# Kernel optimization log

Hardware: AMD Instinct MI355X
Metric: run time of the kernel (lower is better)

## Reference

```python
import jax, jax.numpy as jnp
import numpy as np

B, T, C, H = 2, 2048, 2048, 32
N = C // H  # 64
EPS_GN = 1e-5 * 8 ** 2  # eps = 1e-5 * head_size_divisor**2


def setup_inputs() -> dict:
    key = jax.random.key(0)
    ks = jax.random.split(key, 40)
    p = lambda i, shape, s=1.0: jax.random.normal(ks[i], shape, jnp.float32) * s
    inp = {
        'x': p(0, (B, T, C)),
        'shift_state': jnp.zeros((B, C), jnp.float32),
        'v_first': p(1, (B, T, C)),
        'wkv_state': jnp.zeros((B, H, N, N), jnp.float32),
        # token-shift mix coefficients [1,1,C]
        'x_r': p(2, (1, 1, C), 0.3), 'x_w': p(3, (1, 1, C), 0.3),
        'x_k': p(4, (1, 1, C), 0.3), 'x_v': p(5, (1, 1, C), 0.3),
        'x_a': p(6, (1, 1, C), 0.3), 'x_g': p(7, (1, 1, C), 0.3),
        # decay LoRA
        'w0': p(8, (1, 1, C), 0.5) - 4.0,
        'w1': p(9, (C, 64), 0.02), 'w2': p(10, (64, C), 0.02),
        # in-context-learning-rate LoRA
        'a0': p(11, (1, 1, C), 0.1),
        'a1': p(12, (C, 64), 0.02), 'a2': p(13, (64, C), 0.02),
        # value-mix LoRA
        'v0': p(14, (1, 1, C), 0.1) + 1.0,
        'v1': p(15, (C, 32), 0.02), 'v2': p(16, (32, C), 0.02),
        # gate LoRA
        'g1': p(17, (C, 128), 0.02), 'g2': p(18, (128, C), 0.02),
        'k_k': p(19, (1, 1, C), 0.05) + 0.85,
        'k_a': p(20, (1, 1, C), 0.05) + 1.0,
        'r_k': p(21, (H, N), 0.1),
        # dense projections (applied as x @ W.T like nn.Linear)
        'Wr': p(22, (C, C), 0.02), 'Wk': p(23, (C, C), 0.02),
        'Wv': p(24, (C, C), 0.02), 'Wo': p(25, (C, C), 0.02),
        'ln_w': jnp.ones((C,), jnp.float32),
        'ln_b': jnp.zeros((C,), jnp.float32),
    }
    return inp


def reference(x, shift_state, v_first, wkv_state, x_r, x_w, x_k, x_v, x_a, x_g,
              w0, w1, w2, a0, a1, a2, v0, v1, v2, g1, g2, k_k, k_a, r_k,
              Wr, Wk, Wv, Wo, ln_w, ln_b):
    # token shift: xx[t] = x[t-1] - x[t] (prev from shift_state at t=0)
    xx = jnp.concatenate([shift_state[:, None, :], x[:, :-1]], axis=1) - x
    xr, xw, xk, xv, xa, xg = (x + xx * m for m in (x_r, x_w, x_k, x_v, x_a, x_g))

    r = xr @ Wr.T
    w = -jax.nn.softplus(-(w0 + jnp.tanh(xw @ w1) @ w2)) - 0.5  # log-decay in (-inf,-0.5)
    k = xk @ Wk.T
    v = xv @ Wv.T
    v = v + (v_first - v) * jax.nn.sigmoid(v0 + (xv @ v1) @ v2)  # layer_id > 0 branch
    a = jax.nn.sigmoid(a0 + (xa @ a1) @ a2)
    g = jax.nn.sigmoid(xg @ g1) @ g2

    kk = (k * k_k).reshape(B, T, H, N)
    kk = kk / jnp.maximum(jnp.linalg.norm(kk, axis=-1, keepdims=True), 1e-12)
    kk = kk.reshape(B, T, C)
    k = k * (1.0 + (a - 1.0) * k_a)

    # RWKV-7 generalized delta-rule recurrence (a_in=-kk, b_in=kk*a):
    #   S_t = S_{t-1} * diag(exp(w_t)) + (S_{t-1} a_t) b_t^T + v_t k_t^T ; o_t = S_t r_t
    to_tbhn = lambda z: z.reshape(B, T, H, N).transpose(1, 0, 2, 3)  # [T,B,H,N]
    rs, ws, ks, vs, as_, bs = map(to_tbhn, (r, w, k, v, -kk, kk * a))

    def step(S, ins):  # S: [B,H,N,N] indexed [v_dim, k_dim]
        r_t, w_t, k_t, v_t, a_t, b_t = ins
        sa = jnp.einsum('bhij,bhj->bhi', S, a_t)
        S = (S * jnp.exp(w_t)[:, :, None, :]
             + sa[..., None] * b_t[:, :, None, :]
             + v_t[..., None] * k_t[:, :, None, :])
        o_t = jnp.einsum('bhij,bhj->bhi', S, r_t)
        return S, o_t

    _, o = jax.lax.scan(step, wkv_state, (rs, ws, ks, vs, as_, bs))  # o: [T,B,H,N]
    o = o.transpose(1, 0, 2, 3).reshape(B, T, C)

    # GroupNorm with H groups over channel dim
    og = o.reshape(B, T, H, N)
    mu = og.mean(-1, keepdims=True)
    var = og.var(-1, keepdims=True)
    o = ((og - mu) / jnp.sqrt(var + EPS_GN)).reshape(B, T, C) * ln_w + ln_b

    # bonus term
    rk = (r.reshape(B, T, H, N) * k.reshape(B, T, H, N) * r_k).sum(-1, keepdims=True)
    o = o + (rk * v.reshape(B, T, H, N)).reshape(B, T, C)

    return (o * g) @ Wo.T
```

## Files before the change

kernel.cpp:

```cpp
#include <hip/hip_runtime.h>

#define Bdim 2
#define Tdim 2048
#define Cdim 2048
#define Hdim 32
#define Mdim (Bdim*Tdim)

typedef unsigned short u16;
typedef short bf16x8 __attribute__((ext_vector_type(8)));
typedef short bf16x4 __attribute__((ext_vector_type(4)));
typedef float f32x4 __attribute__((ext_vector_type(4)));

__device__ __forceinline__ u16 f2bf(float f) {
  unsigned u = __float_as_uint(f);
  u = (u + 0x7FFFu + ((u >> 16) & 1u)) >> 16;
  return (u16)u;
}
__device__ __forceinline__ float b2f(u16 h) {
  return __uint_as_float(((unsigned)h) << 16);
}
__device__ __forceinline__ float sigf(float x) { return 1.f / (1.f + expf(-x)); }

__device__ __forceinline__ void gld16(const u16* g, u16* l) {
  __builtin_amdgcn_global_load_lds(
      (const __attribute__((address_space(1))) unsigned int*)g,
      (__attribute__((address_space(3))) unsigned int*)l, 16, 0, 0);
}

__device__ __forceinline__ float dpp_red16(float x) {
  int t = __builtin_amdgcn_mov_dpp(__float_as_int(x), 0x128, 0xF, 0xF, true);
  x += __int_as_float(t);
  t = __builtin_amdgcn_mov_dpp(__float_as_int(x), 0x124, 0xF, 0xF, true);
  x += __int_as_float(t);
  t = __builtin_amdgcn_mov_dpp(__float_as_int(x), 0x122, 0xF, 0xF, true);
  x += __int_as_float(t);
  t = __builtin_amdgcn_mov_dpp(__float_as_int(x), 0x121, 0xF, 0xF, true);
  x += __int_as_float(t);
  return x;
}

__global__ __launch_bounds__(256) void fill_kernel(float* __restrict__ out, float v, int n) {
  int i = blockIdx.x * 256 + threadIdx.x;
  if (i < n) out[i] = v;
}

__global__ __launch_bounds__(256) void prep_kernel(
    const float* __restrict__ x, const float* __restrict__ shift,
    const float* __restrict__ mr, const float* __restrict__ mw,
    const float* __restrict__ mk, const float* __restrict__ mv,
    const float* __restrict__ ma, const float* __restrict__ mg,
    u16* __restrict__ xr_h, u16* __restrict__ xr_l,
    u16* __restrict__ xk_h, u16* __restrict__ xk_l,
    u16* __restrict__ xv_h, u16* __restrict__ xv_l,
    u16* __restrict__ xg_h, u16* __restrict__ xg_l,
    u16* __restrict__ xw, u16* __restrict__ xa)
{
  size_t idx = (size_t)blockIdx.x * 256 + threadIdx.x;
  int c = (int)(idx & (Cdim - 1));
  size_t row = idx >> 11;
  int t = (int)(row & (Tdim - 1));
  int b = (int)(row >> 11);
  float xc = x[idx];
  float xp = (t == 0) ? shift[(size_t)b * Cdim + c] : x[idx - Cdim];
  float xx = xp - xc;

  float vr = xc + xx * mr[c];
  u16 hr = f2bf(vr); xr_h[idx] = hr; xr_l[idx] = f2bf(vr - b2f(hr));
  float vk = xc + xx * mk[c];
  u16 hk = f2bf(vk); xk_h[idx] = hk; xk_l[idx] = f2bf(vk - b2f(hk));
  float vv = xc + xx * mv[c];
  u16 hv = f2bf(vv); xv_h[idx] = hv; xv_l[idx] = f2bf(vv - b2f(hv));
  float vg = xc + xx * mg[c];
  u16 hg = f2bf(vg); xg_h[idx] = hg; xg_l[idx] = f2bf(vg - b2f(hg));

  xw[idx] = f2bf(xc + xx * mw[c]);
  xa[idx] = f2bf(xc + xx * ma[c]);
}

__global__ __launch_bounds__(256) void cast_split_kernel(
    const float* __restrict__ src, u16* __restrict__ hi, u16* __restrict__ lo)
{
  size_t i = (size_t)blockIdx.x * 256 + threadIdx.x;
  float v = src[i];
  u16 h = f2bf(v);
  hi[i] = h;
  lo[i] = f2bf(v - b2f(h));
}

__global__ __launch_bounds__(256) void transpose_pack_kernel(
    const float* __restrict__ src, u16* __restrict__ dst, int K, int Nsrc)
{
  size_t idx = (size_t)blockIdx.x * 256 + threadIdx.x;
  int n = (int)(idx / K);
  int kk = (int)(idx - (size_t)n * K);
  dst[idx] = (n < Nsrc) ? f2bf(src[(size_t)kk * Nsrc + n]) : (u16)0;
}

__global__ __launch_bounds__(256) void transpose_pack_split_kernel(
    const float* __restrict__ src, u16* __restrict__ dh, u16* __restrict__ dl,
    int K, int Nsrc)
{
  size_t idx = (size_t)blockIdx.x * 256 + threadIdx.x;
  int n = (int)(idx / K);
  int kk = (int)(idx - (size_t)n * K);
  float v = (n < Nsrc) ? src[(size_t)kk * Nsrc + n] : 0.f;
  u16 h = f2bf(v);
  dh[idx] = h;
  dl[idx] = f2bf(v - b2f(h));
}


template <int EP>
__device__ __forceinline__ void gemm_plain_body(
    const u16* __restrict__ A, const u16* __restrict__ B, void* __restrict__ Cv,
    const float* __restrict__ bias, const float* __restrict__ aux1,
    const float* __restrict__ aux2, int K, int Nact, int ldC, int act)
{
  __shared__ u16 As[128][32];
  __shared__ u16 Bs[128][32];
  int tid = threadIdx.x;
  int lane = tid & 63, wave = tid >> 6;
  int wm = wave >> 1, wn = wave & 1;
  int bm = blockIdx.x * 128, bn = blockIdx.y * 128;
  f32x4 zero = {0.f, 0.f, 0.f, 0.f};
  f32x4 acc[4][4];
#pragma unroll
  for (int i = 0; i < 4; i++)
#pragma unroll
    for (int j = 0; j < 4; j++) acc[i][j] = zero;
  int srow = tid >> 2;
  int sslot = tid & 3;
  int scol = (sslot ^ (srow & 3)) << 3;
  int dcol = sslot << 3;
  const u16* gA  = A + (size_t)(bm + srow) * K + scol;
  const u16* gA2 = A + (size_t)(bm + 64 + srow) * K + scol;
  const u16* gB  = B + (size_t)(bn + srow) * K + scol;
  const u16* gB2 = B + (size_t)(bn + 64 + srow) * K + scol;
  u16* lA  = &As[srow][dcol];
  u16* lA2 = &As[64 + srow][dcol];
  u16* lB  = &Bs[srow][dcol];
  u16* lB2 = &Bs[64 + srow][dcol];
  int fr = lane & 15;
  int fk = ((lane >> 4) << 3) ^ ((fr & 3) << 3);
  for (int k0 = 0; k0 < K; k0 += 32) {
    __syncthreads();
    gld16(gA + k0, lA);
    gld16(gA2 + k0, lA2);
    gld16(gB + k0, lB);
    gld16(gB2 + k0, lB2);
    __syncthreads();
    bf16x8 af[4], bfv[4];
#pragma unroll
    for (int i = 0; i < 4; i++) af[i] = *(const bf16x8*)&As[wm * 64 + i * 16 + fr][fk];
#pragma unroll
    for (int j = 0; j < 4; j++) bfv[j] = *(const bf16x8*)&Bs[wn * 64 + j * 16 + fr][fk];
#pragma unroll
    for (int i = 0; i < 4; i++)
#pragma unroll
      for (int j = 0; j < 4; j++)
        acc[i][j] = __builtin_amdgcn_mfma_f32_16x16x32_bf16(af[i], bfv[j], acc[i][j], 0, 0, 0);
  }
  int rb = (lane >> 4) << 2;
  int cc = lane & 15;
#pragma unroll
  for (int i = 0; i < 4; i++) {
    int mm = bm + wm * 64 + i * 16 + rb;
#pragma unroll
    for (int j = 0; j < 4; j++) {
      int nn = bn + wn * 64 + j * 16 + cc;
      if (nn < Nact) {
#pragma unroll
        for (int r = 0; r < 4; r++) {
          float val = acc[i][j][r];
          size_t oidx = (size_t)(mm + r) * ldC + nn;
          if (EP == 1) ((u16*)Cv)[oidx] = f2bf(tanhf(val));
          else if (EP == 2) {
            if (act == 1) val = tanhf(val);
            ((u16*)Cv)[oidx] = f2bf(val);
          }
          else if (EP == 3) ((u16*)Cv)[oidx] = f2bf(0.60653065971f * sigf(bias[nn] + val));
          else if (EP == 4) ((float*)Cv)[oidx] = sigf(bias[nn] + val);
          else if (EP == 5) {
            float vraw = aux1[oidx], vf = aux2[oidx];
            ((float*)Cv)[oidx] = vraw + (vf - vraw) * sigf(bias[nn] + val);
          }
        }
      }
    }
  }
}

template <int EP>
__global__ __launch_bounds__(256) void gemm_plain(
    const u16* __restrict__ A, const u16* __restrict__ B, void* __restrict__ C,
    const float* __restrict__ bias, const float* __restrict__ aux1,
    const float* __restrict__ aux2, int K, int Nact, int ldC)
{
  gemm_plain_body<EP>(A, B, C, bias, aux1, aux2, K, Nact, ldC, 0);
}

__global__ __launch_bounds__(256) void lora1_kernel(
    const u16* A0, const u16* A1, const u16* A2,
    const u16* B0, const u16* B1, const u16* B2,
    u16* C0, u16* C1, u16* C2, int N0, int N1, int N2)
{
  int z = blockIdx.z;
  const u16* A = (z == 0) ? A0 : (z == 1) ? A1 : A2;
  const u16* B = (z == 0) ? B0 : (z == 1) ? B1 : B2;
  u16* C      = (z == 0) ? C0 : (z == 1) ? C1 : C2;
  int Nact    = (z == 0) ? N0 : (z == 1) ? N1 : N2;
  int act     = (z == 0) ? 1 : 0;
  gemm_plain_body<2>(A, B, C, nullptr, nullptr, nullptr, 2048, Nact, Nact, act);
}

template <int EP>
__global__ __launch_bounds__(256) void gemm_split(
    const u16* __restrict__ Ah, const u16* __restrict__ Al,
    const u16* __restrict__ Bh, const u16* __restrict__ Bl,
    void* __restrict__ C1, u16* __restrict__ C2, int K, int Nact, int ldC)
{
  __shared__ u16 Ash[128][32];
  __shared__ u16 Asl[128][32];
  __shared__ u16 Bsh[128][32];
  __shared__ u16 Bsl[128][32];
  int tid = threadIdx.x;
  int lane = tid & 63, wave = tid >> 6;
  int wm = wave >> 1, wn = wave & 1;
  int bm = blockIdx.x * 128, bn = blockIdx.y * 128;
  f32x4 zero = {0.f, 0.f, 0.f, 0.f};
  f32x4 acc[4][4];
#pragma unroll
  for (int i = 0; i < 4; i++)
#pragma unroll
    for (int j = 0; j < 4; j++) acc[i][j] = zero;
  int srow = tid >> 2;
  int sslot = tid & 3;
  int scol = (sslot ^ (srow & 3)) << 3;
  int dcol = sslot << 3;
  size_t ga  = (size_t)(bm + srow) * K + scol;
  size_t ga2 = (size_t)(bm + 64 + srow) * K + scol;
  size_t gb  = (size_t)(bn + srow) * K + scol;
  size_t gb2 = (size_t)(bn + 64 + srow) * K + scol;
  u16* lAh = &Ash[srow][dcol];  u16* lAh2 = &Ash[64 + srow][dcol];
  u16* lAl = &Asl[srow][dcol];  u16* lAl2 = &Asl[64 + srow][dcol];
  u16* lBh = &Bsh[srow][dcol];  u16* lBh2 = &Bsh[64 + srow][dcol];
  u16* lBl = &Bsl[srow][dcol];  u16* lBl2 = &Bsl[64 + srow][dcol];
  int fr = lane & 15;
  int fk = ((lane >> 4) << 3) ^ ((fr & 3) << 3);
  for (int k0 = 0; k0 < K; k0 += 32) {
    __syncthreads();
    gld16(Ah + ga + k0, lAh);
    gld16(Ah + ga2 + k0, lAh2);
    gld16(Al + ga + k0, lAl);
    gld16(Al + ga2 + k0, lAl2);
    gld16(Bh + gb + k0, lBh);
    gld16(Bh + gb2 + k0, lBh2);
    gld16(Bl + gb + k0, lBl);
    gld16(Bl + gb2 + k0, lBl2);
    __syncthreads();
    bf16x8 fah[4], fal[4], fbh[4], fbl[4];
#pragma unroll
    for (int i = 0; i < 4; i++) {
      fah[i] = *(const bf16x8*)&Ash[wm * 64 + i * 16 + fr][fk];
      fal[i] = *(const bf16x8*)&Asl[wm * 64 + i * 16 + fr][fk];
    }
#pragma unroll
    for (int j = 0; j < 4; j++) {
      fbh[j] = *(const bf16x8*)&Bsh[wn * 64 + j * 16 + fr][fk];
      fbl[j] = *(const bf16x8*)&Bsl[wn * 64 + j * 16 + fr][fk];
    }
#pragma unroll
    for (int i = 0; i < 4; i++)
#pragma unroll
      for (int j = 0; j < 4; j++) {
        acc[i][j] = __builtin_amdgcn_mfma_f32_16x16x32_bf16(fah[i], fbh[j], acc[i][j], 0, 0, 0);
        acc[i][j] = __builtin_amdgcn_mfma_f32_16x16x32_bf16(fah[i], fbl[j], acc[i][j], 0, 0, 0);
        acc[i][j] = __builtin_amdgcn_mfma_f32_16x16x32_bf16(fal[i], fbh[j], acc[i][j], 0, 0, 0);
      }
  }
  int rb = (lane >> 4) << 2;
  int cc = lane & 15;
#pragma unroll
  for (int i = 0; i < 4; i++) {
    int mm = bm + wm * 64 + i * 16 + rb;
#pragma unroll
    for (int j = 0; j < 4; j++) {
      int nn = bn + wn * 64 + j * 16 + cc;
      if (nn < Nact) {
#pragma unroll
        for (int r = 0; r < 4; r++) {
          float val = acc[i][j][r];
          size_t oidx = (size_t)(mm + r) * ldC + nn;
          if (EP == 0) ((float*)C1)[oidx] = val;
          else {
            float s = sigf(val);
            u16 h = f2bf(s);
            ((u16*)C1)[oidx] = h;
            C2[oidx] = f2bf(s - b2f(h));
          }
        }
      }
    }
  }
}

__global__ __launch_bounds__(256) void post_kernel(
    float* __restrict__ k, const float* __restrict__ a,
    const float* __restrict__ k_k, const float* __restrict__ k_a,
    float* __restrict__ ain, float* __restrict__ bin)
{
  int gid = blockIdx.x * 4 + (threadIdx.x >> 6);
  int lane = threadIdx.x & 63;
  int m = gid >> 5, h = gid & 31;
  int c = h * 64 + lane;
  size_t idx = (size_t)m * Cdim + c;

  float kr = k[idx];
  float av = a[idx];

  float kkv = kr * k_k[c];
  float ss = kkv * kkv;
#pragma unroll
  for (int off = 32; off; off >>= 1) ss += __shfl_xor(ss, off);
  float kkn = kkv / fmaxf(sqrtf(ss), 1e-12f);

  ain[idx] = -kkn;
  bin[idx] = kkn * av;
  k[idx] = kr * (1.f + (av - 1.f) * k_a[c]);
}

__global__ __launch_bounds__(64) void scan_kernel(
    const float* __restrict__ r, const u16* __restrict__ ew,
    const float* __restrict__ k, const float* __restrict__ v,
    const float* __restrict__ ain, const float* __restrict__ bin,
    const float* __restrict__ S0, float* __restrict__ o)
{
  int bh = blockIdx.x & 63;
  int rg = blockIdx.x >> 6;
  int lane = threadIdx.x;
  int c16 = lane & 15;
  int lr = lane >> 4;
  int i = rg * 4 + lr;
  int cb = (bh & 31) * 64;
  size_t mbase = (size_t)(bh >> 5) * Tdim;

  float s[4];
  {
    const float* sp = S0 + (size_t)bh * 4096 + (size_t)i * 64 + c16 * 4;
#pragma unroll
    for (int j = 0; j < 4; j++) s[j] = sp[j];
  }

  f32x4 aA, kA, bA, rA;  bf16x4 eA;  float vA;
  f32x4 aB, kB, bB, rB;  bf16x4 eB;  float vB;
  f32x4 aC, kC, bC, rC;  bf16x4 eC;  float vC;
  f32x4 aD, kD, bD, rD;  bf16x4 eD;  float vD;

#define PRE(tt, P) { \
  size_t vb_ = (mbase + (size_t)(tt)) * Cdim + cb; \
  a##P = *(const f32x4*)(ain + vb_ + c16 * 4); \
  k##P = *(const f32x4*)(k + vb_ + c16 * 4); \
  b##P = *(const f32x4*)(bin + vb_ + c16 * 4); \
  r##P = *(const f32x4*)(r + vb_ + c16 * 4); \
  e##P = *(const bf16x4*)(ew + vb_ + c16 * 4); \
  v##P = v[vb_ + i]; }

#define COMP(tt, P) { \
  float p0_ = s[0] * a##P[0] + s[1] * a##P[1]; \
  float p1_ = s[2] * a##P[2] + s[3] * a##P[3]; \
  float p_ = dpp_red16(p0_ + p1_); \
  float oL_ = 0.f, oH_ = 0.f; \
  _Pragma("unroll") \
  for (int j = 0; j < 2; j++) { \
    float sn0_ = s[j]     * b2f((u16)e##P[j])     + p_ * b##P[j]     + v##P * k##P[j]; \
    float sn1_ = s[2 + j] * b2f((u16)e##P[2 + j]) + p_ * b##P[2 + j] + v##P * k##P[2 + j]; \
    s[j] = sn0_; s[2 + j] = sn1_; \
    oL_ += sn0_ * r##P[j]; oH_ += sn1_ * r##P[2 + j]; \
  } \
  float oo_ = dpp_red16(oL_ + oH_); \
  if (c16 == 0) o[(mbase + (size_t)(tt)) * Cdim + cb + i] = oo_; \
  __builtin_amdgcn_sched_barrier(0); }

  PRE(0, A)
  PRE(1, B)
  PRE(2, C)
  for (int t = 0; t < Tdim - 4; t += 4) {
    PRE(t + 3, D)
    COMP(t, A)
    PRE(t + 4, A)
    COMP(t + 1, B)
    PRE(t + 5, B)
    COMP(t + 2, C)
    PRE(t + 6, C)
    COMP(t + 3, D)
  }
  PRE(Tdim - 1, D)
  COMP(Tdim - 4, A)
  COMP(Tdim - 3, B)
  COMP(Tdim - 2, C)
  COMP(Tdim - 1, D)
#undef PRE
#undef COMP
}

__global__ __launch_bounds__(256) void gn_kernel(
    const float* __restrict__ o_raw, const float* __restrict__ r,
    const float* __restrict__ k, const float* __restrict__ v,
    const float* __restrict__ g, const float* __restrict__ rkw,
    const float* __restrict__ ln_w, const float* __restrict__ ln_b,
    u16* __restrict__ og_h, u16* __restrict__ og_l)
{
  int gid = blockIdx.x * 4 + (threadIdx.x >> 6);
  int lane = threadIdx.x & 63;
  int m = gid >> 5, h = gid & 31;
  int c = h * 64 + lane;
  size_t idx = (size_t)m * Cdim + c;

  float ov = o_raw[idx];
  float rv = r[idx], kv = k[idx], vv = v[idx];
  float rk = rv * kv * rkw[c];

  float s1 = ov, s2 = ov * ov, s3 = rk;
#pragma unroll
  for (int off = 32; off; off >>= 1) {
    s1 += __shfl_xor(s1, off);
    s2 += __shfl_xor(s2, off);
    s3 += __shfl_xor(s3, off);
  }
  float mu = s1 * (1.f / 64.f);
  float var = s2 * (1.f / 64.f) - mu * mu;
  float xh = (ov - mu) * rsqrtf(var + 6.4e-4f);
  float gn = xh * ln_w[c] + ln_b[c];
  float outp = (gn + s3 * vv) * g[idx];
  u16 hh = f2bf(outp);
  og_h[idx] = hh;
  og_l[idx] = f2bf(outp - b2f(hh));
}

extern "C" void kernel_launch(void* const* d_in, const int* in_sizes, int n_in,
                              void* d_out, int out_size, void* d_ws, size_t ws_size,
                              hipStream_t stream) {
  const float* x      = (const float*)d_in[0];
  const float* shiftS = (const float*)d_in[1];
  const float* vfirst = (const float*)d_in[2];
  const float* wkv0   = (const float*)d_in[3];
  const float* x_r = (const float*)d_in[4];
  const float* x_w = (const float*)d_in[5];
  const float* x_k = (const float*)d_in[6];
  const float* x_v = (const float*)d_in[7];
  const float* x_a = (const float*)d_in[8];
  const float* x_g = (const float*)d_in[9];
  const float* w0 = (const float*)d_in[10];
  const float* w1 = (const float*)d_in[11];
  const float* w2 = (const float*)d_in[12];
  const float* a0 = (const float*)d_in[13];
  const float* a1 = (const float*)d_in[14];
  const float* a2 = (const float*)d_in[15];
  const float* v0 = (const float*)d_in[16];
  const float* v1 = (const float*)d_in[17];
  const float* v2 = (const float*)d_in[18];
  const float* g1 = (const float*)d_in[19];
  const float* g2 = (const float*)d_in[20];
  const float* k_k = (const float*)d_in[21];
  const float* k_a = (const float*)d_in[22];
  const float* r_k = (const float*)d_in[23];
  const float* Wr = (const float*)d_in[24];
  const float* Wk = (const float*)d_in[25];
  const float* Wv = (const float*)d_in[26];
  const float* Wo = (const float*)d_in[27];
  const float* ln_w = (const float*)d_in[28];
  const float* ln_b = (const float*)d_in[29];
  (void)in_sizes; (void)n_in;

  const size_t MC = (size_t)Mdim * Cdim;
  const size_t CC = (size_t)Cdim * Cdim;
  const size_t SLOT = MC * 2;

  char* cur = (char*)d_ws;
  auto alloc = [&](size_t bytes) -> void* {
    void* p = cur;
    cur += (bytes + 255) & ~(size_t)255;
    return p;
  };

  char* X = (char*)alloc(13 * SLOT);
  u16* xr_h = (u16*)(X + 0 * SLOT);
  u16* xr_l = (u16*)(X + 1 * SLOT);
  u16* xk_h = (u16*)(X + 2 * SLOT);
  u16* xk_l = (u16*)(X + 3 * SLOT);
  u16* xv_h = (u16*)(X + 4 * SLOT);
  u16* xv_l = (u16*)(X + 5 * SLOT);
  u16* xw   = (u16*)(X + 6 * SLOT);
  u16* xa   = (u16*)(X + 7 * SLOT);
  u16* xg_h = (u16*)(X + 8 * SLOT);
  u16* xg_l = (u16*)(X + 9 * SLOT);
  float* r_f32 = (float*)(X + 8 * SLOT);
  float* k_f32 = (float*)(X + 0 * SLOT);
  float* v_f32 = (float*)(X + 2 * SLOT);
  float* a_f32 = (float*)(X + 10 * SLOT);
  u16*   ew_bf = (u16*)(X + 12 * SLOT);
  float* ain_f = (float*)(X + 4 * SLOT);
  float* bin_f = (float*)(X + 6 * SLOT);
  float* o_f32 = (float*)(X + 10 * SLOT);
  float* g_f32 = (float*)(X + 6 * SLOT);
  u16*   og_h  = (u16*)(X + 4 * SLOT);
  u16*   og_l  = (u16*)(X + 5 * SLOT);

  u16* Wh = (u16*)alloc(CC * 2);
  u16* Wl = (u16*)alloc(CC * 2);

  u16* w1t = (u16*)alloc((size_t)128 * 2048 * 2);
  u16* a1t = (u16*)alloc((size_t)128 * 2048 * 2);
  u16* v1t = (u16*)alloc((size_t)128 * 2048 * 2);
  u16* g1t_h = (u16*)alloc((size_t)128 * 2048 * 2);
  u16* g1t_l = (u16*)alloc((size_t)128 * 2048 * 2);
  u16* w2t = (u16*)alloc((size_t)2048 * 64 * 2);
  u16* a2t = (u16*)alloc((size_t)2048 * 64 * 2);
  u16* v2t = (u16*)alloc((size_t)2048 * 32 * 2);
  u16* g2t_h = (u16*)alloc((size_t)2048 * 128 * 2);
  u16* g2t_l = (u16*)alloc((size_t)2048 * 128 * 2);
  u16* hb_w = (u16*)alloc((size_t)Mdim * 64 * 2);
  u16* hb_a = (u16*)alloc((size_t)Mdim * 64 * 2);
  u16* hb_v = (u16*)alloc((size_t)Mdim * 32 * 2);
  u16* sig_h = (u16*)alloc((size_t)Mdim * 128 * 2);
  u16* sig_l = (u16*)alloc((size_t)Mdim * 128 * 2);

  size_t required = (size_t)(cur - (char*)d_ws);
  if (ws_size < required) {
    fill_kernel<<<(out_size + 255) / 256, 256, 0, stream>>>(
        (float*)d_out, (float)(ws_size >> 20), out_size);
    return;
  }

  prep_kernel<<<(int)(MC / 256), 256, 0, stream>>>(
      x, shiftS, x_r, x_w, x_k, x_v, x_a, x_g,
      xr_h, xr_l, xk_h, xk_l, xv_h, xv_l, xg_h, xg_l, xw, xa);

  transpose_pack_kernel<<<1024, 256, 0, stream>>>(w1, w1t, 2048, 64);
  transpose_pack_kernel<<<1024, 256, 0, stream>>>(a1, a1t, 2048, 64);
  transpose_pack_kernel<<<1024, 256, 0, stream>>>(v1, v1t, 2048, 32);
  transpose_pack_split_kernel<<<1024, 256, 0, stream>>>(g1, g1t_h, g1t_l, 2048, 128);
  transpose_pack_kernel<<<512, 256, 0, stream>>>(w2, w2t, 64, 2048);
  transpose_pack_kernel<<<512, 256, 0, stream>>>(a2, a2t, 64, 2048);
  transpose_pack_kernel<<<256, 256, 0, stream>>>(v2, v2t, 32, 2048);
  transpose_pack_split_kernel<<<1024, 256, 0, stream>>>(g2, g2t_h, g2t_l, 128, 2048);

  dim3 gL1(Mdim / 128, 1, 3);
  lora1_kernel<<<gL1, 256, 0, stream>>>(xw, xa, xv_h, w1t, a1t, v1t,
                                        hb_w, hb_a, hb_v, 64, 64, 32);
  dim3 gL1g(Mdim / 128, 1);
  gemm_split<1><<<gL1g, 256, 0, stream>>>(xg_h, xg_l, g1t_h, g1t_l,
                                          sig_h, sig_l, 2048, 128, 128);

  dim3 gBig(Mdim / 128, Cdim / 128);
  cast_split_kernel<<<(int)(CC / 256), 256, 0, stream>>>(Wr, Wh, Wl);
  gemm_split<0><<<gBig, 256, 0, stream>>>(xr_h, xr_l, Wh, Wl, r_f32, nullptr, Cdim, Cdim, Cdim);
  cast_split_kernel<<<(int)(CC / 256), 256, 0, stream>>>(Wk, Wh, Wl);
  gemm_split<0><<<gBig, 256, 0, stream>>>(xk_h, xk_l, Wh, Wl, k_f32, nullptr, Cdim, Cdim, Cdim);
  cast_split_kernel<<<(int)(CC / 256), 256, 0, stream>>>(Wv, Wh, Wl);
  gemm_split<0><<<gBig, 256, 0, stream>>>(xv_h, xv_l, Wh, Wl, v_f32, nullptr, Cdim, Cdim, Cdim);

  gemm_plain<3><<<gBig, 256, 0, stream>>>(hb_w, w2t, ew_bf, w0, nullptr, nullptr, 64, Cdim, Cdim);
  gemm_plain<4><<<gBig, 256, 0, stream>>>(hb_a, a2t, a_f32, a0, nullptr, nullptr, 64, Cdim, Cdim);
  gemm_plain<5><<<gBig, 256, 0, stream>>>(hb_v, v2t, v_f32, v0, v_f32, vfirst, 32, Cdim, Cdim);

  post_kernel<<<(Mdim * Hdim) / 4, 256, 0, stream>>>(
      k_f32, a_f32, k_k, k_a, ain_f, bin_f);

  scan_kernel<<<1024, 64, 0, stream>>>(
      r_f32, ew_bf, k_f32, v_f32, ain_f, bin_f, wkv0, o_f32);

  gemm_split<0><<<gBig, 256, 0, stream>>>(sig_h, sig_l, g2t_h, g2t_l,
                                          g_f32, nullptr, 128, Cdim, Cdim);

  gn_kernel<<<(Mdim * Hdim) / 4, 256, 0, stream>>>(
      o_f32, r_f32, k_f32, v_f32, g_f32, r_k, ln_w, ln_b, og_h, og_l);

  cast_split_kernel<<<(int)(CC / 256), 256, 0, stream>>>(Wo, Wh, Wl);
  gemm_split<0><<<gBig, 256, 0, stream>>>(og_h, og_l, Wh, Wl,
                                          (float*)d_out, nullptr, Cdim, Cdim, Cdim);
}
```

Baseline: 1.142 ms.

## Double-buffer GEMM LDS tiles and split scan rows across more waves

Both GEMM kernels now use double-buffered shared-memory tiles, so the next K-slice is loaded while MFMAs run on the current one. This halves the barriers per iteration and doubles LDS use per block. The WKV scan now gives each wave 2 state rows instead of 4, with 2 columns per lane, and launches twice as many blocks. The aim is to shorten the per-step serial dependency chain and raise parallelism for the latency-bound scan, at the cost of an extra cross-half shuffle per reduction and more redundant input loads.

```diff
diff --git a/kernel.cpp b/kernel.cpp
--- a/kernel.cpp
+++ b/kernel.cpp
@@ -8,7 +8,7 @@
 
 typedef unsigned short u16;
 typedef short bf16x8 __attribute__((ext_vector_type(8)));
-typedef short bf16x4 __attribute__((ext_vector_type(4)));
+typedef float f32x2 __attribute__((ext_vector_type(2)));
 typedef float f32x4 __attribute__((ext_vector_type(4)));
 
 __device__ __forceinline__ u16 f2bf(float f) {
@@ -116,8 +116,8 @@
     const float* __restrict__ bias, const float* __restrict__ aux1,
     const float* __restrict__ aux2, int K, int Nact, int ldC, int act)
 {
-  __shared__ u16 As[128][32];
-  __shared__ u16 Bs[128][32];
+  __shared__ u16 As[2][128][32];
+  __shared__ u16 Bs[2][128][32];
   int tid = threadIdx.x;
   int lane = tid & 63, wave = tid >> 6;
   int wm = wave >> 1, wn = wave & 1;
@@ -136,30 +136,34 @@
   const u16* gA2 = A + (size_t)(bm + 64 + srow) * K + scol;
   const u16* gB  = B + (size_t)(bn + srow) * K + scol;
   const u16* gB2 = B + (size_t)(bn + 64 + srow) * K + scol;
-  u16* lA  = &As[srow][dcol];
-  u16* lA2 = &As[64 + srow][dcol];
-  u16* lB  = &Bs[srow][dcol];
-  u16* lB2 = &Bs[64 + srow][dcol];
   int fr = lane & 15;
   int fk = ((lane >> 4) << 3) ^ ((fr & 3) << 3);
+
+#define STAGEP(buf, kk) { \
+  gld16(gA + (kk), &As[buf][srow][dcol]); \
+  gld16(gA2 + (kk), &As[buf][64 + srow][dcol]); \
+  gld16(gB + (kk), &Bs[buf][srow][dcol]); \
+  gld16(gB2 + (kk), &Bs[buf][64 + srow][dcol]); }
+
+  STAGEP(0, 0)
+  __syncthreads();
+  int cur = 0;
   for (int k0 = 0; k0 < K; k0 += 32) {
-    __syncthreads();
-    gld16(gA + k0, lA);
-    gld16(gA2 + k0, lA2);
-    gld16(gB + k0, lB);
-    gld16(gB2 + k0, lB2);
-    __syncthreads();
+    if (k0 + 32 < K) STAGEP(cur ^ 1, k0 + 32)
     bf16x8 af[4], bfv[4];
 #pragma unroll
-    for (int i = 0; i < 4; i++) af[i] = *(const bf16x8*)&As[wm * 64 + i * 16 + fr][fk];
-#pragma unroll
-    for (int j = 0; j < 4; j++) bfv[j] = *(const bf16x8*)&Bs[wn * 64 + j * 16 + fr][fk];
+    for (int i = 0; i < 4; i++) af[i] = *(const bf16x8*)&As[cur][wm * 64 + i * 16 + fr][fk];
+#pragma unroll
+    for (int j = 0; j < 4; j++) bfv[j] = *(const bf16x8*)&Bs[cur][wn * 64 + j * 16 + fr][fk];
 #pragma unroll
     for (int i = 0; i < 4; i++)
 #pragma unroll
       for (int j = 0; j < 4; j++)
         acc[i][j] = __builtin_amdgcn_mfma_f32_16x16x32_bf16(af[i], bfv[j], acc[i][j], 0, 0, 0);
-  }
+    __syncthreads();
+    cur ^= 1;
+  }
+#undef STAGEP
   int rb = (lane >> 4) << 2;
   int cc = lane & 15;
 #pragma unroll
@@ -219,10 +223,10 @@
     const u16* __restrict__ Bh, const u16* __restrict__ Bl,
     void* __restrict__ C1, u16* __restrict__ C2, int K, int Nact, int ldC)
 {
-  __shared__ u16 Ash[128][32];
-  __shared__ u16 Asl[128][32];
-  __shared__ u16 Bsh[128][32];
-  __shared__ u16 Bsl[128][32];
+  __shared__ u16 Ash[2][128][32];
+  __shared__ u16 Asl[2][128][32];
+  __shared__ u16 Bsh[2][128][32];
+  __shared__ u16 Bsl[2][128][32];
   int tid = threadIdx.x;
   int lane = tid & 63, wave = tid >> 6;
   int wm = wave >> 1, wn = wave & 1;
@@ -241,33 +245,34 @@
   size_t ga2 = (size_t)(bm + 64 + srow) * K + scol;
   size_t gb  = (size_t)(bn + srow) * K + scol;
   size_t gb2 = (size_t)(bn + 64 + srow) * K + scol;
-  u16* lAh = &Ash[srow][dcol];  u16* lAh2 = &Ash[64 + srow][dcol];
-  u16* lAl = &Asl[srow][dcol];  u16* lAl2 = &Asl[64 + srow][dcol];
-  u16* lBh = &Bsh[srow][dcol];  u16* lBh2 = &Bsh[64 + srow][dcol];
-  u16* lBl = &Bsl[srow][dcol];  u16* lBl2 = &Bsl[64 + srow][dcol];
   int fr = lane & 15;
   int fk = ((lane >> 4) << 3) ^ ((fr & 3) << 3);
+
+#define STAGES(buf, kk) { \
+  gld16(Ah + ga + (kk), &Ash[buf][srow][dcol]); \
+  gld16(Ah + ga2 + (kk), &Ash[buf][64 + srow][dcol]); \
+  gld16(Al + ga + (kk), &Asl[buf][srow][dcol]); \
+  gld16(Al + ga2 + (kk), &Asl[buf][64 + srow][dcol]); \
+  gld16(Bh + gb + (kk), &Bsh[buf][srow][dcol]); \
+  gld16(Bh + gb2 + (kk), &Bsh[buf][64 + srow][dcol]); \
+  gld16(Bl + gb + (kk), &Bsl[buf][srow][dcol]); \
+  gld16(Bl + gb2 + (kk), &Bsl[buf][64 + srow][dcol]); }
+
+  STAGES(0, 0)
+  __syncthreads();
+  int cur = 0;
   for (int k0 = 0; k0 < K; k0 += 32) {
-    __syncthreads();
-    gld16(Ah + ga + k0, lAh);
-    gld16(Ah + ga2 + k0, lAh2);
-    gld16(Al + ga + k0, lAl);
-    gld16(Al + ga2 + k0, lAl2);
-    gld16(Bh + gb + k0, lBh);
-    gld16(Bh + gb2 + k0, lBh2);
-    gld16(Bl + gb + k0, lBl);
-    gld16(Bl + gb2 + k0, lBl2);
-    __syncthreads();
+    if (k0 + 32 < K) STAGES(cur ^ 1, k0 + 32)
     bf16x8 fah[4], fal[4], fbh[4], fbl[4];
 #pragma unroll
     for (int i = 0; i < 4; i++) {
-      fah[i] = *(const bf16x8*)&Ash[wm * 64 + i * 16 + fr][fk];
-      fal[i] = *(const bf16x8*)&Asl[wm * 64 + i * 16 + fr][fk];
+      fah[i] = *(const bf16x8*)&Ash[cur][wm * 64 + i * 16 + fr][fk];
+      fal[i] = *(const bf16x8*)&Asl[cur][wm * 64 + i * 16 + fr][fk];
     }
 #pragma unroll
     for (int j = 0; j < 4; j++) {
-      fbh[j] = *(const bf16x8*)&Bsh[wn * 64 + j * 16 + fr][fk];
-      fbl[j] = *(const bf16x8*)&Bsl[wn * 64 + j * 16 + fr][fk];
+      fbh[j] = *(const bf16x8*)&Bsh[cur][wn * 64 + j * 16 + fr][fk];
+      fbl[j] = *(const bf16x8*)&Bsl[cur][wn * 64 + j * 16 + fr][fk];
     }
 #pragma unroll
     for (int i = 0; i < 4; i++)
@@ -277,7 +282,10 @@
         acc[i][j] = __builtin_amdgcn_mfma_f32_16x16x32_bf16(fah[i], fbl[j], acc[i][j], 0, 0, 0);
         acc[i][j] = __builtin_amdgcn_mfma_f32_16x16x32_bf16(fal[i], fbh[j], acc[i][j], 0, 0, 0);
       }
-  }
+    __syncthreads();
+    cur ^= 1;
+  }
+#undef STAGES
   int rb = (lane >> 4) << 2;
   int cc = lane & 15;
 #pragma unroll
@@ -338,47 +346,45 @@
   int bh = blockIdx.x & 63;
   int rg = blockIdx.x >> 6;
   int lane = threadIdx.x;
-  int c16 = lane & 15;
-  int lr = lane >> 4;
-  int i = rg * 4 + lr;
+  int jci = (lane & 15) | ((lane >> 1) & 16);
+  int lr = (lane >> 4) & 1;
+  int i = rg * 2 + lr;
   int cb = (bh & 31) * 64;
   size_t mbase = (size_t)(bh >> 5) * Tdim;
 
-  float s[4];
+  float s0, s1;
   {
-    const float* sp = S0 + (size_t)bh * 4096 + (size_t)i * 64 + c16 * 4;
-#pragma unroll
-    for (int j = 0; j < 4; j++) s[j] = sp[j];
-  }
-
-  f32x4 aA, kA, bA, rA;  bf16x4 eA;  float vA;
-  f32x4 aB, kB, bB, rB;  bf16x4 eB;  float vB;
-  f32x4 aC, kC, bC, rC;  bf16x4 eC;  float vC;
-  f32x4 aD, kD, bD, rD;  bf16x4 eD;  float vD;
+    const float* sp = S0 + (size_t)bh * 4096 + (size_t)i * 64 + jci * 2;
+    s0 = sp[0]; s1 = sp[1];
+  }
+
+  f32x2 aA, kA, bA, rA;  unsigned eA;  float vA;
+  f32x2 aB, kB, bB, rB;  unsigned eB;  float vB;
+  f32x2 aC, kC, bC, rC;  unsigned eC;  float vC;
+  f32x2 aD, kD, bD, rD;  unsigned eD;  float vD;
 
 #define PRE(tt, P) { \
   size_t vb_ = (mbase + (size_t)(tt)) * Cdim + cb; \
-  a##P = *(const f32x4*)(ain + vb_ + c16 * 4); \
-  k##P = *(const f32x4*)(k + vb_ + c16 * 4); \
-  b##P = *(const f32x4*)(bin + vb_ + c16 * 4); \
-  r##P = *(const f32x4*)(r + vb_ + c16 * 4); \
-  e##P = *(const bf16x4*)(ew + vb_ + c16 * 4); \
+  a##P = *(const f32x2*)(ain + vb_ + jci * 2); \
+  k##P = *(const f32x2*)(k + vb_ + jci * 2); \
+  b##P = *(const f32x2*)(bin + vb_ + jci * 2); \
+  r##P = *(const f32x2*)(r + vb_ + jci * 2); \
+  e##P = *(const unsigned*)(ew + vb_ + jci * 2); \
   v##P = v[vb_ + i]; }
 
 #define COMP(tt, P) { \
-  float p0_ = s[0] * a##P[0] + s[1] * a##P[1]; \
-  float p1_ = s[2] * a##P[2] + s[3] * a##P[3]; \
-  float p_ = dpp_red16(p0_ + p1_); \
-  float oL_ = 0.f, oH_ = 0.f; \
-  _Pragma("unroll") \
-  for (int j = 0; j < 2; j++) { \
-    float sn0_ = s[j]     * b2f((u16)e##P[j])     + p_ * b##P[j]     + v##P * k##P[j]; \
-    float sn1_ = s[2 + j] * b2f((u16)e##P[2 + j]) + p_ * b##P[2 + j] + v##P * k##P[2 + j]; \
-    s[j] = sn0_; s[2 + j] = sn1_; \
-    oL_ += sn0_ * r##P[j]; oH_ += sn1_ * r##P[2 + j]; \
-  } \
-  float oo_ = dpp_red16(oL_ + oH_); \
-  if (c16 == 0) o[(mbase + (size_t)(tt)) * Cdim + cb + i] = oo_; \
+  float p_ = s0 * a##P[0] + s1 * a##P[1]; \
+  p_ = dpp_red16(p_); \
+  p_ += __shfl_xor(p_, 32); \
+  float e0_ = b2f((u16)(e##P & 0xFFFFu)); \
+  float e1_ = b2f((u16)(e##P >> 16)); \
+  float sn0_ = s0 * e0_ + p_ * b##P[0] + v##P * k##P[0]; \
+  float sn1_ = s1 * e1_ + p_ * b##P[1] + v##P * k##P[1]; \
+  s0 = sn0_; s1 = sn1_; \
+  float oo_ = sn0_ * r##P[0] + sn1_ * r##P[1]; \
+  oo_ = dpp_red16(oo_); \
+  oo_ += __shfl_xor(oo_, 32); \
+  if (jci == 0) o[(mbase + (size_t)(tt)) * Cdim + cb + i] = oo_; \
   __builtin_amdgcn_sched_barrier(0); }
 
   PRE(0, A)
@@ -567,7 +573,7 @@
   post_kernel<<<(Mdim * Hdim) / 4, 256, 0, stream>>>(
       k_f32, a_f32, k_k, k_a, ain_f, bin_f);
 
-  scan_kernel<<<1024, 64, 0, stream>>>(
+  scan_kernel<<<2048, 64, 0, stream>>>(
       r_f32, ew_bf, k_f32, v_f32, ain_f, bin_f, wkv0, o_f32);
 
   gemm_split<0><<<gBig, 256, 0, stream>>>(sig_h, sig_l, g2t_h, g2t_l,
```

Result: slower. 1.409 ms (+23.4%).
